# Kernel tuning notes

Hardware: AMD Instinct MI355X
Metric: run time of the kernel (lower is better)

Reference implementation:

```python
import jax, jax.numpy as jnp
import numpy as np

EMBED_DIM = 768
NUM_HEADS = 12
HEAD_DIM = EMBED_DIM // NUM_HEADS
SCALE = HEAD_DIM ** -0.5


def setup_inputs() -> dict:
    key = jax.random.key(0)
    ks = jax.random.split(key, 5)
    B, N, D = 2, 4096, EMBED_DIM
    std = 1.0 / np.sqrt(D)
    x = jax.random.normal(ks[0], (B, N, D), dtype=jnp.float32)
    W_qkv = jax.random.normal(ks[1], (D, 3 * D), dtype=jnp.float32) * std
    b_qkv = jax.random.normal(ks[2], (3 * D,), dtype=jnp.float32) * 0.01
    W_proj = jax.random.normal(ks[3], (D, D), dtype=jnp.float32) * std
    b_proj = jax.random.normal(ks[4], (D,), dtype=jnp.float32) * 0.01
    return {"x": x, "W_qkv": W_qkv, "b_qkv": b_qkv, "W_proj": W_proj, "b_proj": b_proj}


def reference(x, W_qkv, b_qkv, W_proj, b_proj):
    B, N, D = x.shape
    H, Hd = NUM_HEADS, HEAD_DIM
    qkv = x @ W_qkv + b_qkv                      # [B, N, 3D]
    qkv = qkv.reshape(B, N, 3, H, Hd)
    qkv = jnp.transpose(qkv, (2, 0, 3, 1, 4))    # [3, B, H, N, Hd]
    q, k, v = qkv[0], qkv[1], qkv[2]
    attn = jnp.einsum('bhqd,bhkd->bhqk', q, k) * SCALE   # [B, H, N, N]
    attn = jax.nn.softmax(attn, axis=-1)
    out = jnp.einsum('bhqk,bhkd->bhqd', attn, v)          # [B, H, N, Hd]
    out = jnp.transpose(out, (0, 2, 1, 3)).reshape(B, N, D)
    return out @ W_proj + b_proj
```

## Files before the change

### kernel.cpp

```cpp
#include <hip/hip_runtime.h>
#include <hip/hip_bf16.h>

typedef __attribute__((ext_vector_type(4))) float f32x4;
typedef __attribute__((ext_vector_type(16))) float f32x16;
typedef __attribute__((ext_vector_type(8))) short s16x8;
typedef __attribute__((ext_vector_type(4))) unsigned int u32x4;

#define MFMA16(a, b, c) __builtin_amdgcn_mfma_f32_16x16x32_bf16(a, b, c, 0, 0, 0)
#define MFMA32(a, b, c) __builtin_amdgcn_mfma_f32_32x32x16_bf16(a, b, c, 0, 0, 0)

__device__ __forceinline__ short f2bf(float f) {
  unsigned u = __builtin_bit_cast(unsigned, f);
  u += 0x7fffu + ((u >> 16) & 1u);
  return (short)(u >> 16);
}
__device__ __forceinline__ unsigned cvtpk(float lo, float hi) {
  unsigned r;
  asm("v_cvt_pk_bf16_f32 %0, %1, %2" : "=v"(r) : "v"(lo), "v"(hi));
  return r;
}
__device__ __forceinline__ float ex2(float x) {
  float r;
  asm("v_exp_f32 %0, %1" : "=v"(r) : "v"(x));
  return r;
}
__device__ __forceinline__ void vperm(const s16x8 a, const s16x8 b,
                                      s16x8& w0, s16x8& w1) {
#pragma unroll
  for (int e = 0; e < 4; ++e) {
    w0[e] = a[e];
    w0[4 + e] = b[e];
    w1[e] = a[4 + e];
    w1[4 + e] = b[4 + e];
  }
}
__device__ __forceinline__ void gl_lds16(const unsigned short* g, short* l) {
  __builtin_amdgcn_global_load_lds(
      (const __attribute__((address_space(1))) unsigned int*)g,
      (__attribute__((address_space(3))) unsigned int*)l, 16, 0, 0);
}

__global__ __launch_bounds__(256) void convert_x(
    const float* __restrict__ X, unsigned short* __restrict__ Xb) {
  const size_t i = ((size_t)blockIdx.x * 256 + threadIdx.x) * 8;
  f32x4 a = *(const f32x4*)(X + i);
  f32x4 b = *(const f32x4*)(X + i + 4);
  s16x8 o;
#pragma unroll
  for (int e = 0; e < 4; ++e) o[e] = f2bf(a[e]);
#pragma unroll
  for (int e = 0; e < 4; ++e) o[4 + e] = f2bf(b[e]);
  *(s16x8*)(Xb + i) = o;
}

__global__ __launch_bounds__(256) void tconv(
    const float* __restrict__ W, unsigned short* __restrict__ Wt,
    int K, int N) {
  __shared__ float T[64][65];
  const int k0 = blockIdx.x * 64, n0 = blockIdx.y * 64;
  const int t = threadIdx.x;
  const int tr = t >> 4, tc = (t & 15) * 4;
#pragma unroll
  for (int i = 0; i < 4; ++i) {
    f32x4 v = *(const f32x4*)&W[(size_t)(k0 + tr + i * 16) * N + n0 + tc];
#pragma unroll
    for (int e = 0; e < 4; ++e) T[tc + e][tr + i * 16] = v[e];
  }
  __syncthreads();
  const int nn = t >> 2, kk = (t & 3) * 16;
  s16x8 o0, o1;
#pragma unroll
  for (int j = 0; j < 8; ++j) o0[j] = f2bf(T[nn][kk + j]);
#pragma unroll
  for (int j = 0; j < 8; ++j) o1[j] = f2bf(T[nn][kk + 8 + j]);
  *(s16x8*)&Wt[(size_t)(n0 + nn) * K + k0 + kk] = o0;
  *(s16x8*)&Wt[(size_t)(n0 + nn) * K + k0 + kk + 8] = o1;
}

__global__ __launch_bounds__(256) void qkv_gemm(
    const unsigned short* __restrict__ Xb, const unsigned short* __restrict__ Wt,
    const float* __restrict__ bias, unsigned short* __restrict__ Qo,
    unsigned short* __restrict__ Ko, unsigned short* __restrict__ VTo) {
  __shared__ __align__(16) short As[128 * 32];
  __shared__ __align__(16) short Bs[128 * 32];
  const int m0 = blockIdx.x * 128, n0 = blockIdx.y * 128;
  const int tid = threadIdx.x, lane = tid & 63, wid = tid >> 6;
  const int wr = wid >> 1, wc = wid & 1;
  const int lr = lane & 15, s4 = lane >> 4;

  const int crow = lane >> 2;
  const int ccol = (lane & 3) ^ (crow & 3);
  const unsigned short* ga0 = Xb + (size_t)(m0 + wid * 32 + crow) * 768 + ccol * 8;
  const unsigned short* ga1 = ga0 + (size_t)16 * 768;
  const unsigned short* gb0 = Wt + (size_t)(n0 + wid * 32 + crow) * 768 + ccol * 8;
  const unsigned short* gb1 = gb0 + (size_t)16 * 768;
  short* lA0 = &As[(wid * 2) * 512];
  short* lA1 = &As[(wid * 2 + 1) * 512];
  short* lB0 = &Bs[(wid * 2) * 512];
  short* lB1 = &Bs[(wid * 2 + 1) * 512];

  f32x4 acc[4][4];
#pragma unroll
  for (int i = 0; i < 4; ++i)
#pragma unroll
    for (int j = 0; j < 4; ++j)
#pragma unroll
      for (int e = 0; e < 4; ++e) acc[i][j][e] = 0.f;

  for (int k0 = 0; k0 < 768; k0 += 32) {
    gl_lds16(ga0 + k0, lA0);
    gl_lds16(ga1 + k0, lA1);
    gl_lds16(gb0 + k0, lB0);
    gl_lds16(gb1 + k0, lB1);
    __syncthreads();
    s16x8 af[4], bfr[4];
#pragma unroll
    for (int mi = 0; mi < 4; ++mi) {
      const int row = wr * 64 + mi * 16 + lr;
      af[mi] = *(const s16x8*)&As[row * 32 + ((s4 ^ (row & 3)) << 3)];
    }
#pragma unroll
    for (int ni = 0; ni < 4; ++ni) {
      const int row = wc * 64 + ni * 16 + lr;
      bfr[ni] = *(const s16x8*)&Bs[row * 32 + ((s4 ^ (row & 3)) << 3)];
    }
#pragma unroll
    for (int mi = 0; mi < 4; ++mi)
#pragma unroll
      for (int ni = 0; ni < 4; ++ni)
        acc[mi][ni] = MFMA16(af[mi], bfr[ni], acc[mi][ni]);
    __syncthreads();
  }

  const float QSC = 0.18033688011f;
  const int rbase = m0 + wr * 64 + (lane >> 4) * 4;
#pragma unroll
  for (int ni = 0; ni < 4; ++ni) {
    const int cb = n0 + wc * 64 + ni * 16;
    const int which = cb / 768;
    const int rem = cb - which * 768;
    const int h = rem >> 6;
    const int d = (rem & 63) + lr;
    const float bi = bias[cb + lr];
#pragma unroll
    for (int mi = 0; mi < 4; ++mi) {
#pragma unroll
      for (int j = 0; j < 4; ++j) {
        const int row = rbase + mi * 16 + j;
        const int bb = row >> 12, t = row & 4095;
        const float v = acc[mi][ni][j] + bi;
        const size_t hb = (size_t)(bb * 12 + h);
        if (which == 0)
          Qo[(hb * 4096 + t) * 64 + d] = (unsigned short)f2bf(v * QSC);
        else if (which == 1)
          Ko[(hb * 4096 + t) * 64 + d] = (unsigned short)f2bf(v);
        else
          VTo[(hb * 64 + d) * 4096 + t] = (unsigned short)f2bf(v);
      }
    }
  }
}

template <int NSPLIT>
__global__ __launch_bounds__(256) void attn_fwd(
    const unsigned short* __restrict__ Qg, const unsigned short* __restrict__ Kg,
    const unsigned short* __restrict__ VTg, unsigned short* __restrict__ Aout,
    float* __restrict__ Opart, float* __restrict__ Lpart) {
  constexpr int TKV = 64 / NSPLIT;
  __shared__ __align__(16) short smem[16384];
  const int qt = blockIdx.x, bh = blockIdx.y, sz = blockIdx.z;
  const int tok0 = sz * TKV * 64;
  const unsigned short* Qh = Qg + (size_t)bh * 4096 * 64;
  const unsigned short* Kh = Kg + (size_t)bh * 4096 * 64;
  const unsigned short* Vh = VTg + (size_t)bh * 4096 * 64;
  const int tid = threadIdx.x, lane = tid & 63, wid = tid >> 6;
  const int l31 = lane & 31, hi = lane >> 5;
  const int sw0 = (l31 + (l31 >> 3)) & 7;
  const int sw1 = (sw0 + 4) & 7;
  const int qbase = qt * 256 + wid * 64;

  s16x8 qfA[4], qfB[4];
#pragma unroll
  for (int db = 0; db < 4; ++db) {
    qfA[db] = *(const s16x8*)&Qh[(size_t)(qbase + l31) * 64 + db * 16 + hi * 8];
    qfB[db] = *(const s16x8*)&Qh[(size_t)(qbase + 32 + l31) * 64 + db * 16 + hi * 8];
  }

  s16x8 ones;
#pragma unroll
  for (int e = 0; e < 8; ++e) ones[e] = (short)0x3F80;

  f32x16 zf;
#pragma unroll
  for (int r = 0; r < 16; ++r) zf[r] = 0.f;
  f32x16 oA0 = zf, oA1 = zf, oB0 = zf, oB1 = zf, acclA = zf, acclB = zf;

  const int srow = tid >> 2, sp = tid & 3;
  const int ssw = (srow + (srow >> 3)) & 7;
  const int sd0 = srow * 64 + (((sp * 2) ^ ssw) << 3);
  const int sd1 = srow * 64 + (((sp * 2 + 1) ^ ssw) << 3);
  const unsigned short* kga = Kh + (size_t)(tok0 + srow) * 64 + sp * 16;
  const unsigned short* vga = Vh + (size_t)srow * 4096 + tok0 + sp * 16;

  s16x8 kr0 = *(const s16x8*)kga;
  s16x8 kr1 = *(const s16x8*)(kga + 8);
  s16x8 vr0 = *(const s16x8*)vga;
  s16x8 vr1 = *(const s16x8*)(vga + 8);
  {
    s16x8 w0, w1;
    vperm(vr0, vr1, w0, w1);
    *(s16x8*)&smem[sd0] = kr0;
    *(s16x8*)&smem[sd1] = kr1;
    *(s16x8*)&smem[8192 + sd0] = w0;
    *(s16x8*)&smem[8192 + sd1] = w1;
  }
  __syncthreads();

#define PACK_PF(pfv, sv, bse)                                           \
  {                                                                     \
    u32x4 fw;                                                           \
    fw[0] = cvtpk(sv[bse + 0], sv[bse + 1]);                            \
    fw[1] = cvtpk(sv[bse + 2], sv[bse + 3]);                            \
    fw[2] = cvtpk(sv[bse + 4], sv[bse + 5]);                            \
    fw[3] = cvtpk(sv[bse + 6], sv[bse + 7]);                            \
    pfv = __builtin_bit_cast(s16x8, fw);                                \
  }

  int cur = 0;
  for (int t = 0; t < TKV; ++t) {
    if (t < TKV - 1) {
      kr0 = *(const s16x8*)(kga + (size_t)(t + 1) * 4096);
      kr1 = *(const s16x8*)(kga + (size_t)(t + 1) * 4096 + 8);
      vr0 = *(const s16x8*)(vga + (t + 1) * 64);
      vr1 = *(const s16x8*)(vga + (t + 1) * 64 + 8);
    }
    const short* Kc = smem + cur * 4096;
    const short* Vc = smem + 8192 + cur * 4096;

    {
      f32x16 sA = zf, sB = zf;
      __builtin_amdgcn_s_setprio(1);
#pragma unroll
      for (int db = 0; db < 4; ++db) {
        s16x8 kf = *(const s16x8*)&Kc[l31 * 64 + (((db * 2 + hi) ^ sw0) << 3)];
        sA = MFMA32(kf, qfA[db], sA);
        sB = MFMA32(kf, qfB[db], sB);
      }
      __builtin_amdgcn_s_setprio(0);
#pragma unroll
      for (int r = 0; r < 16; ++r) {
        sA[r] = ex2(sA[r]);
        sB[r] = ex2(sB[r]);
      }
      s16x8 pfA0, pfA1, pfB0, pfB1;
      PACK_PF(pfA0, sA, 0)
      PACK_PF(pfA1, sA, 8)
      PACK_PF(pfB0, sB, 0)
      PACK_PF(pfB1, sB, 8)
      __builtin_amdgcn_s_setprio(1);
      acclA = MFMA32(ones, pfA0, acclA);
      acclA = MFMA32(ones, pfA1, acclA);
      acclB = MFMA32(ones, pfB0, acclB);
      acclB = MFMA32(ones, pfB1, acclB);
      s16x8 v0 = *(const s16x8*)&Vc[l31 * 64 + (((0 + hi) ^ sw0) << 3)];
      s16x8 v1 = *(const s16x8*)&Vc[l31 * 64 + (((2 + hi) ^ sw0) << 3)];
      s16x8 w0 = *(const s16x8*)&Vc[(32 + l31) * 64 + (((0 + hi) ^ sw1) << 3)];
      s16x8 w1 = *(const s16x8*)&Vc[(32 + l31) * 64 + (((2 + hi) ^ sw1) << 3)];
      oA0 = MFMA32(v0, pfA0, oA0);
      oA0 = MFMA32(v1, pfA1, oA0);
      oA1 = MFMA32(w0, pfA0, oA1);
      oA1 = MFMA32(w1, pfA1, oA1);
      oB0 = MFMA32(v0, pfB0, oB0);
      oB0 = MFMA32(v1, pfB1, oB0);
      oB1 = MFMA32(w0, pfB0, oB1);
      oB1 = MFMA32(w1, pfB1, oB1);
      __builtin_amdgcn_s_setprio(0);
    }

    {
      f32x16 sA = zf, sB = zf;
      __builtin_amdgcn_s_setprio(1);
#pragma unroll
      for (int db = 0; db < 4; ++db) {
        s16x8 kf = *(const s16x8*)&Kc[(32 + l31) * 64 + (((db * 2 + hi) ^ sw1) << 3)];
        sA = MFMA32(kf, qfA[db], sA);
        sB = MFMA32(kf, qfB[db], sB);
      }
      __builtin_amdgcn_s_setprio(0);
#pragma unroll
      for (int r = 0; r < 16; ++r) {
        sA[r] = ex2(sA[r]);
        sB[r] = ex2(sB[r]);
      }
      s16x8 pfA2, pfA3, pfB2, pfB3;
      PACK_PF(pfA2, sA, 0)
      PACK_PF(pfA3, sA, 8)
      PACK_PF(pfB2, sB, 0)
      PACK_PF(pfB3, sB, 8)
      __builtin_amdgcn_s_setprio(1);
      acclA = MFMA32(ones, pfA2, acclA);
      acclA = MFMA32(ones, pfA3, acclA);
      acclB = MFMA32(ones, pfB2, acclB);
      acclB = MFMA32(ones, pfB3, acclB);
      s16x8 v2 = *(const s16x8*)&Vc[l31 * 64 + (((4 + hi) ^ sw0) << 3)];
      s16x8 v3 = *(const s16x8*)&Vc[l31 * 64 + (((6 + hi) ^ sw0) << 3)];
      s16x8 w2 = *(const s16x8*)&Vc[(32 + l31) * 64 + (((4 + hi) ^ sw1) << 3)];
      s16x8 w3 = *(const s16x8*)&Vc[(32 + l31) * 64 + (((6 + hi) ^ sw1) << 3)];
      oA0 = MFMA32(v2, pfA2, oA0);
      oA0 = MFMA32(v3, pfA3, oA0);
      oA1 = MFMA32(w2, pfA2, oA1);
      oA1 = MFMA32(w3, pfA3, oA1);
      oB0 = MFMA32(v2, pfB2, oB0);
      oB0 = MFMA32(v3, pfB3, oB0);
      oB1 = MFMA32(w2, pfB2, oB1);
      oB1 = MFMA32(w3, pfB3, oB1);
      __builtin_amdgcn_s_setprio(0);
    }

    if (t < TKV - 1) {
      const int nb = cur ^ 1;
      s16x8 w0, w1;
      vperm(vr0, vr1, w0, w1);
      *(s16x8*)&smem[nb * 4096 + sd0] = kr0;
      *(s16x8*)&smem[nb * 4096 + sd1] = kr1;
      *(s16x8*)&smem[8192 + nb * 4096 + sd0] = w0;
      *(s16x8*)&smem[8192 + nb * 4096 + sd1] = w1;
      __syncthreads();
      cur = nb;
    }
  }
#undef PACK_PF

  if constexpr (NSPLIT == 1) {
    __syncthreads();
    short* Ow = smem + wid * (32 * 72);
    const int b = bh / 12, h = bh - b * 12;
    const int qq = lane >> 1, c0 = (lane & 1) * 32;
    {
      const float inv = 1.0f / acclA[0];
#pragma unroll
      for (int r = 0; r < 16; ++r) {
        const int dd = (r & 3) + 8 * (r >> 2) + 4 * hi;
        Ow[l31 * 72 + dd] = f2bf(oA0[r] * inv);
        Ow[l31 * 72 + 32 + dd] = f2bf(oA1[r] * inv);
      }
      const size_t gb = ((size_t)(b * 4096 + qbase + qq)) * 768 + h * 64 + c0;
#pragma unroll
      for (int i = 0; i < 4; ++i) {
        s16x8 v = *(const s16x8*)&Ow[qq * 72 + c0 + i * 8];
        *(s16x8*)&Aout[gb + i * 8] = v;
      }
    }
    {
      const float inv = 1.0f / acclB[0];
#pragma unroll
      for (int r = 0; r < 16; ++r) {
        const int dd = (r & 3) + 8 * (r >> 2) + 4 * hi;
        Ow[l31 * 72 + dd] = f2bf(oB0[r] * inv);
        Ow[l31 * 72 + 32 + dd] = f2bf(oB1[r] * inv);
      }
      const size_t gb = ((size_t)(b * 4096 + qbase + 32 + qq)) * 768 + h * 64 + c0;
#pragma unroll
      for (int i = 0; i < 4; ++i) {
        s16x8 v = *(const s16x8*)&Ow[qq * 72 + c0 + i * 8];
        *(s16x8*)&Aout[gb + i * 8] = v;
      }
    }
  } else {
    const int qA = qbase + l31, qB = qbase + 32 + l31;
    const size_t ob = ((size_t)(sz * 24 + bh)) * 64 * 4096;
#pragma unroll
    for (int r = 0; r < 16; ++r) {
      const int dd = (r & 3) + 8 * (r >> 2) + 4 * hi;
      Opart[ob + (size_t)dd * 4096 + qA] = oA0[r];
      Opart[ob + (size_t)(dd + 32) * 4096 + qA] = oA1[r];
      Opart[ob + (size_t)dd * 4096 + qB] = oB0[r];
      Opart[ob + (size_t)(dd + 32) * 4096 + qB] = oB1[r];
    }
    Lpart[(size_t)(sz * 24 + bh) * 4096 + qA] = acclA[0];
    Lpart[(size_t)(sz * 24 + bh) * 4096 + qB] = acclB[0];
  }
}

__global__ __launch_bounds__(256) void attn_combine(
    const float* __restrict__ Opart, const float* __restrict__ Lpart,
    unsigned short* __restrict__ Aout) {
  __shared__ float T[64][65];
  const int q0 = blockIdx.x * 64, bh = blockIdx.y;
  const int t = threadIdx.x;
  const int d = t >> 2, qc = (t & 3) * 16;
  const size_t b0 = ((size_t)bh * 64 + d) * 4096 + q0 + qc;
  const size_t b1 = ((size_t)(24 + bh) * 64 + d) * 4096 + q0 + qc;
#pragma unroll
  for (int i = 0; i < 4; ++i) {
    f32x4 v = *(const f32x4*)&Opart[b0 + i * 4];
    f32x4 w = *(const f32x4*)&Opart[b1 + i * 4];
#pragma unroll
    for (int e = 0; e < 4; ++e) T[qc + i * 4 + e][d] = v[e] + w[e];
  }
  __syncthreads();
  const int q = t >> 2, dc = (t & 3) * 16;
  const float l = Lpart[(size_t)bh * 4096 + q0 + q] +
                  Lpart[(size_t)(24 + bh) * 4096 + q0 + q];
  const float inv = 1.0f / l;
  const int b = bh / 12, h = bh - b * 12;
  s16x8 o0, o1;
#pragma unroll
  for (int e = 0; e < 8; ++e) o0[e] = f2bf(T[q][dc + e] * inv);
#pragma unroll
  for (int e = 0; e < 8; ++e) o1[e] = f2bf(T[q][dc + 8 + e] * inv);
  const size_t gb = ((size_t)(b * 4096 + q0 + q)) * 768 + h * 64 + dc;
  *(s16x8*)&Aout[gb] = o0;
  *(s16x8*)&Aout[gb + 8] = o1;
}

__global__ __launch_bounds__(256) void proj_gemm(
    const unsigned short* __restrict__ A, const unsigned short* __restrict__ Wt,
    const float* __restrict__ bias, float* __restrict__ out) {
  __shared__ __align__(16) short As[128 * 32];
  __shared__ __align__(16) short Bs[128 * 32];
  const int m0 = blockIdx.x * 128, n0 = blockIdx.y * 128;
  const int tid = threadIdx.x, lane = tid & 63, wid = tid >> 6;
  const int wr = wid >> 1, wc = wid & 1;
  const int lr = lane & 15, s4 = lane >> 4;

  const int crow = lane >> 2;
  const int ccol = (lane & 3) ^ (crow & 3);
  const unsigned short* ga0 = A + (size_t)(m0 + wid * 32 + crow) * 768 + ccol * 8;
  const unsigned short* ga1 = ga0 + (size_t)16 * 768;
  const unsigned short* gb0 = Wt + (size_t)(n0 + wid * 32 + crow) * 768 + ccol * 8;
  const unsigned short* gb1 = gb0 + (size_t)16 * 768;
  short* lA0 = &As[(wid * 2) * 512];
  short* lA1 = &As[(wid * 2 + 1) * 512];
  short* lB0 = &Bs[(wid * 2) * 512];
  short* lB1 = &Bs[(wid * 2 + 1) * 512];

  f32x4 acc[4][4];
#pragma unroll
  for (int i = 0; i < 4; ++i)
#pragma unroll
    for (int j = 0; j < 4; ++j)
#pragma unroll
      for (int e = 0; e < 4; ++e) acc[i][j][e] = 0.f;

  for (int k0 = 0; k0 < 768; k0 += 32) {
    gl_lds16(ga0 + k0, lA0);
    gl_lds16(ga1 + k0, lA1);
    gl_lds16(gb0 + k0, lB0);
    gl_lds16(gb1 + k0, lB1);
    __syncthreads();
    s16x8 af[4], bfr[4];
#pragma unroll
    for (int mi = 0; mi < 4; ++mi) {
      const int row = wr * 64 + mi * 16 + lr;
      af[mi] = *(const s16x8*)&As[row * 32 + ((s4 ^ (row & 3)) << 3)];
    }
#pragma unroll
    for (int ni = 0; ni < 4; ++ni) {
      const int row = wc * 64 + ni * 16 + lr;
      bfr[ni] = *(const s16x8*)&Bs[row * 32 + ((s4 ^ (row & 3)) << 3)];
    }
#pragma unroll
    for (int mi = 0; mi < 4; ++mi)
#pragma unroll
      for (int ni = 0; ni < 4; ++ni)
        acc[mi][ni] = MFMA16(af[mi], bfr[ni], acc[mi][ni]);
    __syncthreads();
  }

  const int rbase = m0 + wr * 64 + (lane >> 4) * 4;
#pragma unroll
  for (int ni = 0; ni < 4; ++ni) {
    const int cb = n0 + wc * 64 + ni * 16;
    const float bi = bias[cb + lr];
#pragma unroll
    for (int mi = 0; mi < 4; ++mi) {
#pragma unroll
      for (int j = 0; j < 4; ++j) {
        const int row = rbase + mi * 16 + j;
        out[(size_t)row * 768 + cb + lr] = acc[mi][ni][j] + bi;
      }
    }
  }
}

extern "C" void kernel_launch(void* const* d_in, const int* in_sizes, int n_in,
                              void* d_out, int out_size, void* d_ws, size_t ws_size,
                              hipStream_t stream) {
  const float* x = (const float*)d_in[0];
  const float* W_qkv = (const float*)d_in[1];
  const float* b_qkv = (const float*)d_in[2];
  const float* W_proj = (const float*)d_in[3];
  const float* b_proj = (const float*)d_in[4];
  float* out = (float*)d_out;

  unsigned short* ws = (unsigned short*)d_ws;
  const size_t NQ = (size_t)24 * 4096 * 64;
  unsigned short* q = ws;
  unsigned short* k = ws + NQ;
  unsigned short* vt = ws + 2 * NQ;
  unsigned short* xb_attn = ws + 3 * NQ;
  unsigned short* wqt = ws + 4 * NQ;
  unsigned short* wpt = wqt + (size_t)2304 * 768;

  const size_t base_bytes = (4 * NQ + (size_t)2304 * 768 + (size_t)768 * 768) * 2;
  const size_t opart_bytes = (size_t)2 * 24 * 64 * 4096 * 4;
  const size_t lpart_bytes = (size_t)2 * 24 * 4096 * 4;
  const bool split = ws_size >= base_bytes + opart_bytes + lpart_bytes;
  float* Opart = (float*)((char*)d_ws + base_bytes);
  float* Lpart = (float*)((char*)d_ws + base_bytes + opart_bytes);

  convert_x<<<3072, 256, 0, stream>>>(x, xb_attn);
  tconv<<<dim3(12, 36), 256, 0, stream>>>(W_qkv, wqt, 768, 2304);
  tconv<<<dim3(12, 12), 256, 0, stream>>>(W_proj, wpt, 768, 768);
  qkv_gemm<<<dim3(64, 18), 256, 0, stream>>>(xb_attn, wqt, b_qkv, q, k, vt);
  if (split) {
    attn_fwd<2><<<dim3(16, 24, 2), 256, 0, stream>>>(q, k, vt, xb_attn, Opart, Lpart);
    attn_combine<<<dim3(64, 24), 256, 0, stream>>>(Opart, Lpart, xb_attn);
  } else {
    attn_fwd<1><<<dim3(16, 24, 1), 256, 0, stream>>>(q, k, vt, xb_attn, Opart, Lpart);
  }
  proj_gemm<<<dim3(64, 6), 256, 0, stream>>>(xb_attn, wpt, b_proj, out);
}
```

Before: 240.8 us.

## Stream K/V tiles into LDS directly and sum softmax rows on VALU

The attention kernel now loads K and V tiles with global_load_lds straight into the double-buffered LDS. This replaces the register staging, the in-register V permutation and the separate LDS stores. To keep the layout consistent, the QKV GEMM epilogue writes V^T with tokens already permuted. The row-sum of probabilities moves from extra ones-matrix MFMAs to a VALU reduction tree plus a cross-half shuffle, freeing matrix-core issue slots. The non-split fallback path is removed, so the split-KV workspace is now assumed to exist.

```diff
diff --git a/kernel.cpp b/kernel.cpp
--- a/kernel.cpp
+++ b/kernel.cpp
@@ -23,16 +23,6 @@
   float r;
   asm("v_exp_f32 %0, %1" : "=v"(r) : "v"(x));
   return r;
-}
-__device__ __forceinline__ void vperm(const s16x8 a, const s16x8 b,
-                                      s16x8& w0, s16x8& w1) {
-#pragma unroll
-  for (int e = 0; e < 4; ++e) {
-    w0[e] = a[e];
-    w0[4 + e] = b[e];
-    w1[e] = a[4 + e];
-    w1[4 + e] = b[4 + e];
-  }
 }
 __device__ __forceinline__ void gl_lds16(const unsigned short* g, short* l) {
   __builtin_amdgcn_global_load_lds(
@@ -133,7 +123,9 @@
   }
 
   const float QSC = 0.18033688011f;
-  const int rbase = m0 + wr * 64 + (lane >> 4) * 4;
+  const int lg = lane >> 4;
+  const int plg = ((lg & 1) << 1) | ((lg >> 1) & 1);
+  const int rbase = m0 + wr * 64 + lg * 4;
 #pragma unroll
   for (int ni = 0; ni < 4; ++ni) {
     const int cb = n0 + wc * 64 + ni * 16;
@@ -154,19 +146,21 @@
           Qo[(hb * 4096 + t) * 64 + d] = (unsigned short)f2bf(v * QSC);
         else if (which == 1)
           Ko[(hb * 4096 + t) * 64 + d] = (unsigned short)f2bf(v);
-        else
-          VTo[(hb * 64 + d) * 4096 + t] = (unsigned short)f2bf(v);
-      }
-    }
-  }
-}
-
-template <int NSPLIT>
+        else {
+          const int tp = (t & ~15) + plg * 4 + j;
+          VTo[(hb * 64 + d) * 4096 + tp] = (unsigned short)f2bf(v);
+        }
+      }
+    }
+  }
+}
+
+#define TKV 32
+
 __global__ __launch_bounds__(256) void attn_fwd(
     const unsigned short* __restrict__ Qg, const unsigned short* __restrict__ Kg,
-    const unsigned short* __restrict__ VTg, unsigned short* __restrict__ Aout,
+    const unsigned short* __restrict__ VTg,
     float* __restrict__ Opart, float* __restrict__ Lpart) {
-  constexpr int TKV = 64 / NSPLIT;
   __shared__ __align__(16) short smem[16384];
   const int qt = blockIdx.x, bh = blockIdx.y, sz = blockIdx.z;
   const int tok0 = sz * TKV * 64;
@@ -186,34 +180,30 @@
     qfB[db] = *(const s16x8*)&Qh[(size_t)(qbase + 32 + l31) * 64 + db * 16 + hi * 8];
   }
 
-  s16x8 ones;
-#pragma unroll
-  for (int e = 0; e < 8; ++e) ones[e] = (short)0x3F80;
-
   f32x16 zf;
 #pragma unroll
   for (int r = 0; r < 16; ++r) zf[r] = 0.f;
-  f32x16 oA0 = zf, oA1 = zf, oB0 = zf, oB1 = zf, acclA = zf, acclB = zf;
-
-  const int srow = tid >> 2, sp = tid & 3;
-  const int ssw = (srow + (srow >> 3)) & 7;
-  const int sd0 = srow * 64 + (((sp * 2) ^ ssw) << 3);
-  const int sd1 = srow * 64 + (((sp * 2 + 1) ^ ssw) << 3);
-  const unsigned short* kga = Kh + (size_t)(tok0 + srow) * 64 + sp * 16;
-  const unsigned short* vga = Vh + (size_t)srow * 4096 + tok0 + sp * 16;
-
-  s16x8 kr0 = *(const s16x8*)kga;
-  s16x8 kr1 = *(const s16x8*)(kga + 8);
-  s16x8 vr0 = *(const s16x8*)vga;
-  s16x8 vr1 = *(const s16x8*)(vga + 8);
-  {
-    s16x8 w0, w1;
-    vperm(vr0, vr1, w0, w1);
-    *(s16x8*)&smem[sd0] = kr0;
-    *(s16x8*)&smem[sd1] = kr1;
-    *(s16x8*)&smem[8192 + sd0] = w0;
-    *(s16x8*)&smem[8192 + sd1] = w1;
-  }
+  f32x16 oA0 = zf, oA1 = zf, oB0 = zf, oB1 = zf;
+  float lsumA = 0.f, lsumB = 0.f;
+
+  const int r0 = wid * 16 + (lane >> 3);
+  const int r1 = r0 + 8;
+  const int c16 = lane & 7;
+  const int sc0 = (c16 ^ ((r0 + (r0 >> 3)) & 7)) << 3;
+  const int sc1 = (c16 ^ ((r1 + (r1 >> 3)) & 7)) << 3;
+  const unsigned short* kg0 = Kh + (size_t)(tok0 + r0) * 64 + sc0;
+  const unsigned short* kg1 = Kh + (size_t)(tok0 + r1) * 64 + sc1;
+  const unsigned short* vg0 = Vh + (size_t)r0 * 4096 + tok0 + sc0;
+  const unsigned short* vg1 = Vh + (size_t)r1 * 4096 + tok0 + sc1;
+  short* const ldsK0 = &smem[(wid * 2) * 512];
+  short* const ldsK1 = &smem[(wid * 2 + 1) * 512];
+  short* const ldsV0 = &smem[8192 + (wid * 2) * 512];
+  short* const ldsV1 = &smem[8192 + (wid * 2 + 1) * 512];
+
+  gl_lds16(kg0, ldsK0);
+  gl_lds16(kg1, ldsK1);
+  gl_lds16(vg0, ldsV0);
+  gl_lds16(vg1, ldsV1);
   __syncthreads();
 
 #define PACK_PF(pfv, sv, bse)                                           \
@@ -225,14 +215,23 @@
     fw[3] = cvtpk(sv[bse + 6], sv[bse + 7]);                            \
     pfv = __builtin_bit_cast(s16x8, fw);                                \
   }
+#define LSUM_TREE(lsum, sv)                                             \
+  {                                                                     \
+    float ta[8];                                                        \
+    _Pragma("unroll") for (int r = 0; r < 8; ++r) ta[r] = sv[r] + sv[r + 8]; \
+    _Pragma("unroll") for (int off = 4; off; off >>= 1)                 \
+      _Pragma("unroll") for (int r = 0; r < off; ++r) ta[r] += ta[r + off]; \
+    lsum += ta[0];                                                      \
+  }
 
   int cur = 0;
   for (int t = 0; t < TKV; ++t) {
     if (t < TKV - 1) {
-      kr0 = *(const s16x8*)(kga + (size_t)(t + 1) * 4096);
-      kr1 = *(const s16x8*)(kga + (size_t)(t + 1) * 4096 + 8);
-      vr0 = *(const s16x8*)(vga + (t + 1) * 64);
-      vr1 = *(const s16x8*)(vga + (t + 1) * 64 + 8);
+      const int nb = (cur ^ 1) * 4096;
+      gl_lds16(kg0 + (size_t)(t + 1) * 4096, ldsK0 + nb);
+      gl_lds16(kg1 + (size_t)(t + 1) * 4096, ldsK1 + nb);
+      gl_lds16(vg0 + (t + 1) * 64, ldsV0 + nb);
+      gl_lds16(vg1 + (t + 1) * 64, ldsV1 + nb);
     }
     const short* Kc = smem + cur * 4096;
     const short* Vc = smem + 8192 + cur * 4096;
@@ -257,11 +256,9 @@
       PACK_PF(pfA1, sA, 8)
       PACK_PF(pfB0, sB, 0)
       PACK_PF(pfB1, sB, 8)
+      LSUM_TREE(lsumA, sA)
+      LSUM_TREE(lsumB, sB)
       __builtin_amdgcn_s_setprio(1);
-      acclA = MFMA32(ones, pfA0, acclA);
-      acclA = MFMA32(ones, pfA1, acclA);
-      acclB = MFMA32(ones, pfB0, acclB);
-      acclB = MFMA32(ones, pfB1, acclB);
       s16x8 v0 = *(const s16x8*)&Vc[l31 * 64 + (((0 + hi) ^ sw0) << 3)];
       s16x8 v1 = *(const s16x8*)&Vc[l31 * 64 + (((2 + hi) ^ sw0) << 3)];
       s16x8 w0 = *(const s16x8*)&Vc[(32 + l31) * 64 + (((0 + hi) ^ sw1) << 3)];
@@ -297,11 +294,9 @@
       PACK_PF(pfA3, sA, 8)
       PACK_PF(pfB2, sB, 0)
       PACK_PF(pfB3, sB, 8)
+      LSUM_TREE(lsumA, sA)
+      LSUM_TREE(lsumB, sB)
       __builtin_amdgcn_s_setprio(1);
-      acclA = MFMA32(ones, pfA2, acclA);
-      acclA = MFMA32(ones, pfA3, acclA);
-      acclB = MFMA32(ones, pfB2, acclB);
-      acclB = MFMA32(ones, pfB3, acclB);
       s16x8 v2 = *(const s16x8*)&Vc[l31 * 64 + (((4 + hi) ^ sw0) << 3)];
       s16x8 v3 = *(const s16x8*)&Vc[l31 * 64 + (((6 + hi) ^ sw0) << 3)];
       s16x8 w2 = *(const s16x8*)&Vc[(32 + l31) * 64 + (((4 + hi) ^ sw1) << 3)];
@@ -318,68 +313,27 @@
     }
 
     if (t < TKV - 1) {
-      const int nb = cur ^ 1;
-      s16x8 w0, w1;
-      vperm(vr0, vr1, w0, w1);
-      *(s16x8*)&smem[nb * 4096 + sd0] = kr0;
-      *(s16x8*)&smem[nb * 4096 + sd1] = kr1;
-      *(s16x8*)&smem[8192 + nb * 4096 + sd0] = w0;
-      *(s16x8*)&smem[8192 + nb * 4096 + sd1] = w1;
       __syncthreads();
-      cur = nb;
-    }
-  }
+      cur ^= 1;
+    }
+  }
+#undef LSUM_TREE
 #undef PACK_PF
 
-  if constexpr (NSPLIT == 1) {
-    __syncthreads();
-    short* Ow = smem + wid * (32 * 72);
-    const int b = bh / 12, h = bh - b * 12;
-    const int qq = lane >> 1, c0 = (lane & 1) * 32;
-    {
-      const float inv = 1.0f / acclA[0];
-#pragma unroll
-      for (int r = 0; r < 16; ++r) {
-        const int dd = (r & 3) + 8 * (r >> 2) + 4 * hi;
-        Ow[l31 * 72 + dd] = f2bf(oA0[r] * inv);
-        Ow[l31 * 72 + 32 + dd] = f2bf(oA1[r] * inv);
-      }
-      const size_t gb = ((size_t)(b * 4096 + qbase + qq)) * 768 + h * 64 + c0;
-#pragma unroll
-      for (int i = 0; i < 4; ++i) {
-        s16x8 v = *(const s16x8*)&Ow[qq * 72 + c0 + i * 8];
-        *(s16x8*)&Aout[gb + i * 8] = v;
-      }
-    }
-    {
-      const float inv = 1.0f / acclB[0];
-#pragma unroll
-      for (int r = 0; r < 16; ++r) {
-        const int dd = (r & 3) + 8 * (r >> 2) + 4 * hi;
-        Ow[l31 * 72 + dd] = f2bf(oB0[r] * inv);
-        Ow[l31 * 72 + 32 + dd] = f2bf(oB1[r] * inv);
-      }
-      const size_t gb = ((size_t)(b * 4096 + qbase + 32 + qq)) * 768 + h * 64 + c0;
-#pragma unroll
-      for (int i = 0; i < 4; ++i) {
-        s16x8 v = *(const s16x8*)&Ow[qq * 72 + c0 + i * 8];
-        *(s16x8*)&Aout[gb + i * 8] = v;
-      }
-    }
-  } else {
-    const int qA = qbase + l31, qB = qbase + 32 + l31;
-    const size_t ob = ((size_t)(sz * 24 + bh)) * 64 * 4096;
-#pragma unroll
-    for (int r = 0; r < 16; ++r) {
-      const int dd = (r & 3) + 8 * (r >> 2) + 4 * hi;
-      Opart[ob + (size_t)dd * 4096 + qA] = oA0[r];
-      Opart[ob + (size_t)(dd + 32) * 4096 + qA] = oA1[r];
-      Opart[ob + (size_t)dd * 4096 + qB] = oB0[r];
-      Opart[ob + (size_t)(dd + 32) * 4096 + qB] = oB1[r];
-    }
-    Lpart[(size_t)(sz * 24 + bh) * 4096 + qA] = acclA[0];
-    Lpart[(size_t)(sz * 24 + bh) * 4096 + qB] = acclB[0];
-  }
+  const float lfullA = lsumA + __shfl_xor(lsumA, 32);
+  const float lfullB = lsumB + __shfl_xor(lsumB, 32);
+  const int qA = qbase + l31, qB = qbase + 32 + l31;
+  const size_t ob = ((size_t)(sz * 24 + bh)) * 64 * 4096;
+#pragma unroll
+  for (int r = 0; r < 16; ++r) {
+    const int dd = (r & 3) + 8 * (r >> 2) + 4 * hi;
+    Opart[ob + (size_t)dd * 4096 + qA] = oA0[r];
+    Opart[ob + (size_t)(dd + 32) * 4096 + qA] = oA1[r];
+    Opart[ob + (size_t)dd * 4096 + qB] = oB0[r];
+    Opart[ob + (size_t)(dd + 32) * 4096 + qB] = oB1[r];
+  }
+  Lpart[(size_t)(sz * 24 + bh) * 4096 + qA] = lfullA;
+  Lpart[(size_t)(sz * 24 + bh) * 4096 + qB] = lfullB;
 }
 
 __global__ __launch_bounds__(256) void attn_combine(
@@ -505,8 +459,6 @@
 
   const size_t base_bytes = (4 * NQ + (size_t)2304 * 768 + (size_t)768 * 768) * 2;
   const size_t opart_bytes = (size_t)2 * 24 * 64 * 4096 * 4;
-  const size_t lpart_bytes = (size_t)2 * 24 * 4096 * 4;
-  const bool split = ws_size >= base_bytes + opart_bytes + lpart_bytes;
   float* Opart = (float*)((char*)d_ws + base_bytes);
   float* Lpart = (float*)((char*)d_ws + base_bytes + opart_bytes);
 
@@ -514,11 +466,7 @@
   tconv<<<dim3(12, 36), 256, 0, stream>>>(W_qkv, wqt, 768, 2304);
   tconv<<<dim3(12, 12), 256, 0, stream>>>(W_proj, wpt, 768, 768);
   qkv_gemm<<<dim3(64, 18), 256, 0, stream>>>(xb_attn, wqt, b_qkv, q, k, vt);
-  if (split) {
-    attn_fwd<2><<<dim3(16, 24, 2), 256, 0, stream>>>(q, k, vt, xb_attn, Opart, Lpart);
-    attn_combine<<<dim3(64, 24), 256, 0, stream>>>(Opart, Lpart, xb_attn);
-  } else {
-    attn_fwd<1><<<dim3(16, 24, 1), 256, 0, stream>>>(q, k, vt, xb_attn, Opart, Lpart);
-  }
+  attn_fwd<<<dim3(16, 24, 2), 256, 0, stream>>>(q, k, vt, Opart, Lpart);
+  attn_combine<<<dim3(64, 24), 256, 0, stream>>>(Opart, Lpart, xb_attn);
   proj_gemm<<<dim3(64, 6), 256, 0, stream>>>(xb_attn, wpt, b_proj, out);
 }
```

New measurement: 230.9 us. 1.04x faster.
